# Kernel optimization log

Hardware: AMD Instinct MI355X
Metric: run time of the kernel (lower is better)

Reference implementation:

```python
import jax, jax.numpy as jnp
import numpy as np

NUM_GRAPHS = 1024  # fill_max for batch ids; fixed num_segments for jit


def setup_inputs() -> dict:
    key = jax.random.key(0)
    k1, k2 = jax.random.split(key)
    N, D = 1000000, 256
    x = jax.random.normal(k1, (N, D), dtype=jnp.float32)
    batch = jnp.sort(jax.random.randint(k2, (N,), 0, NUM_GRAPHS, dtype=jnp.int64))
    return {"input": x, "batch": batch}


def reference(input, batch):
    # per-node L2 norm over feature dim: [N]
    all_norms = jnp.sqrt(jnp.sum(input.astype(jnp.float32) ** 2, axis=1))
    seg = batch.astype(jnp.int32)
    # segment-reduce: sum of norms and node counts per graph, [NUM_GRAPHS]
    norm_sum = jax.ops.segment_sum(all_norms, seg, num_segments=NUM_GRAPHS)
    counts = jax.ops.segment_sum(jnp.ones_like(all_norms), seg, num_segments=NUM_GRAPHS)
    per_graph = jnp.where(counts > 0, norm_sum / counts, 0.0)
    # original loops b in range(batch.max()) -> graphs 0..max-1 only
    bmax = batch.max().astype(jnp.float32)
    mask = jnp.arange(NUM_GRAPHS, dtype=jnp.float32) < bmax
    norm_mean = jnp.sum(per_graph * mask) / (bmax + 1.0)
    # module returns input unchanged; norm_mean is the recorded statistic
    return input, norm_mean
```

## Files before the change

kernel.cpp:

```cpp
#include <hip/hip_runtime.h>

#define NUM_GRAPHS 1024
#define D 256

__global__ void activs_init_kernel(float* __restrict__ sums, float* __restrict__ cnts) {
    int i = blockIdx.x * blockDim.x + threadIdx.x;
    if (i < NUM_GRAPHS) {
        sums[i] = 0.0f;
        cnts[i] = 0.0f;
    }
}

__device__ __forceinline__ float sq4(const float4 v) {
    return v.x * v.x + v.y * v.y + v.z * v.z + v.w * v.w;
}

struct Rows8 {
    float4 v0, v1, v2, v3, v4, v5, v6, v7;
};

__device__ __forceinline__ void load8(Rows8& R, const float* __restrict__ x,
                                      int r, int lane) {
    R.v0 = ((const float4*)(x + (size_t)(r + 0) * D))[lane];
    R.v1 = ((const float4*)(x + (size_t)(r + 1) * D))[lane];
    R.v2 = ((const float4*)(x + (size_t)(r + 2) * D))[lane];
    R.v3 = ((const float4*)(x + (size_t)(r + 3) * D))[lane];
    R.v4 = ((const float4*)(x + (size_t)(r + 4) * D))[lane];
    R.v5 = ((const float4*)(x + (size_t)(r + 5) * D))[lane];
    R.v6 = ((const float4*)(x + (size_t)(r + 6) * D))[lane];
    R.v7 = ((const float4*)(x + (size_t)(r + 7) * D))[lane];
}

__device__ __forceinline__ void store8(const Rows8& R, float* __restrict__ out,
                                       int r, int lane) {
    ((float4*)(out + (size_t)(r + 0) * D))[lane] = R.v0;
    ((float4*)(out + (size_t)(r + 1) * D))[lane] = R.v1;
    ((float4*)(out + (size_t)(r + 2) * D))[lane] = R.v2;
    ((float4*)(out + (size_t)(r + 3) * D))[lane] = R.v3;
    ((float4*)(out + (size_t)(r + 4) * D))[lane] = R.v4;
    ((float4*)(out + (size_t)(r + 5) * D))[lane] = R.v5;
    ((float4*)(out + (size_t)(r + 6) * D))[lane] = R.v6;
    ((float4*)(out + (size_t)(r + 7) * D))[lane] = R.v7;
}

__global__ __launch_bounds__(256) void activs_stream_kernel(
        const float* __restrict__ x, float* __restrict__ out,
        float* __restrict__ norms, int N) {
    const int lane = threadIdx.x & 63;
    const int waveId = (blockIdx.x * blockDim.x + threadIdx.x) >> 6;
    const int totalWaves = (gridDim.x * blockDim.x) >> 6;
    const int stride = totalWaves * 8;

    const int Nq = N & ~7;

    int r = waveId * 8;
    if (r < Nq) {
        Rows8 cur;
        load8(cur, x, r, lane);

        while (true) {
            const int rn = r + stride;
            const bool more = (rn < Nq);
            Rows8 nxt;
            if (more) load8(nxt, x, rn, lane);

            store8(cur, out, r, lane);

            float s0 = sq4(cur.v0), s1 = sq4(cur.v1);
            float s2 = sq4(cur.v2), s3 = sq4(cur.v3);
            float s4 = sq4(cur.v4), s5 = sq4(cur.v5);
            float s6 = sq4(cur.v6), s7 = sq4(cur.v7);
            #pragma unroll
            for (int m = 1; m <= 32; m <<= 1) {
                s0 += __shfl_xor(s0, m, 64);
                s1 += __shfl_xor(s1, m, 64);
                s2 += __shfl_xor(s2, m, 64);
                s3 += __shfl_xor(s3, m, 64);
                s4 += __shfl_xor(s4, m, 64);
                s5 += __shfl_xor(s5, m, 64);
                s6 += __shfl_xor(s6, m, 64);
                s7 += __shfl_xor(s7, m, 64);
            }
            float nv = s0;
            nv = (lane == 1) ? s1 : nv;
            nv = (lane == 2) ? s2 : nv;
            nv = (lane == 3) ? s3 : nv;
            nv = (lane == 4) ? s4 : nv;
            nv = (lane == 5) ? s5 : nv;
            nv = (lane == 6) ? s6 : nv;
            nv = (lane == 7) ? s7 : nv;
            if (lane < 8) norms[r + lane] = sqrtf(nv);

            if (!more) break;
            cur = nxt;
            r = rn;
        }
    }

    if (waveId == 0) {
        for (int t = Nq; t < N; ++t) {
            const float4 v = ((const float4*)(x + (size_t)t * D))[lane];
            ((float4*)(out + (size_t)t * D))[lane] = v;
            float s = sq4(v);
            #pragma unroll
            for (int m = 32; m; m >>= 1) s += __shfl_xor(s, m, 64);
            if (lane == 0) norms[t] = sqrtf(s);
        }
    }
}

__global__ __launch_bounds__(256) void activs_segred_kernel(
        const float* __restrict__ norms, const int* __restrict__ batch,
        float* __restrict__ sums, float* __restrict__ cnts, int N) {
    __shared__ float lsum[NUM_GRAPHS];
    __shared__ float lcnt[NUM_GRAPHS];
    const int tid = threadIdx.x;

    for (int i = tid; i < NUM_GRAPHS; i += 256) {
        lsum[i] = 0.0f;
        lcnt[i] = 0.0f;
    }
    __syncthreads();

    const int base = blockIdx.x * 1024 + tid * 4;
    if (base < N) {
        const float4 nv = *(const float4*)(norms + base);
        const int4 bv = *(const int4*)(batch + base);
        const float n[4] = {nv.x, nv.y, nv.z, nv.w};
        const int b[4] = {bv.x, bv.y, bv.z, bv.w};
        int seg = b[0];
        float rs = n[0], rc = 1.0f;
        #pragma unroll
        for (int k = 1; k < 4; ++k) {
            if (b[k] == seg) { rs += n[k]; rc += 1.0f; }
            else {
                atomicAdd(&lsum[seg], rs);
                atomicAdd(&lcnt[seg], rc);
                seg = b[k]; rs = n[k]; rc = 1.0f;
            }
        }
        atomicAdd(&lsum[seg], rs);
        atomicAdd(&lcnt[seg], rc);
    }
    __syncthreads();

    for (int i = tid; i < NUM_GRAPHS; i += 256) {
        if (lcnt[i] != 0.0f) {
            atomicAdd(&sums[i], lsum[i]);
            atomicAdd(&cnts[i], lcnt[i]);
        }
    }
}

__global__ __launch_bounds__(256) void activs_fused_kernel(
        const float* __restrict__ x, const int* __restrict__ batch,
        float* __restrict__ out, float* __restrict__ sums,
        float* __restrict__ cnts, int N) {
    const int lane = threadIdx.x & 63;
    const int waveId = (blockIdx.x * blockDim.x + threadIdx.x) >> 6;
    const int totalWaves = (gridDim.x * blockDim.x) >> 6;
    const int stride = totalWaves * 8;
    const int Nq = N & ~7;

    int r = waveId * 8;
    if (r < Nq) {
        Rows8 cur;
        load8(cur, x, r, lane);
        int4 w0 = ((const int4*)(batch + r))[0];
        int4 w1 = ((const int4*)(batch + r))[1];

        while (true) {
            const int rn = r + stride;
            const bool more = (rn < Nq);
            Rows8 nxt;
            int4 nw0, nw1;
            if (more) {
                load8(nxt, x, rn, lane);
                nw0 = ((const int4*)(batch + rn))[0];
                nw1 = ((const int4*)(batch + rn))[1];
            }
            store8(cur, out, r, lane);

            float s0 = sq4(cur.v0), s1 = sq4(cur.v1);
            float s2 = sq4(cur.v2), s3 = sq4(cur.v3);
            float s4 = sq4(cur.v4), s5 = sq4(cur.v5);
            float s6 = sq4(cur.v6), s7 = sq4(cur.v7);
            #pragma unroll
            for (int m = 1; m <= 32; m <<= 1) {
                s0 += __shfl_xor(s0, m, 64);
                s1 += __shfl_xor(s1, m, 64);
                s2 += __shfl_xor(s2, m, 64);
                s3 += __shfl_xor(s3, m, 64);
                s4 += __shfl_xor(s4, m, 64);
                s5 += __shfl_xor(s5, m, 64);
                s6 += __shfl_xor(s6, m, 64);
                s7 += __shfl_xor(s7, m, 64);
            }

            if (lane == 0) {
                const float n[8] = {sqrtf(s0), sqrtf(s1), sqrtf(s2), sqrtf(s3),
                                    sqrtf(s4), sqrtf(s5), sqrtf(s6), sqrtf(s7)};
                const int b[8] = {w0.x, w0.y, w0.z, w0.w, w1.x, w1.y, w1.z, w1.w};
                int seg = b[0];
                float rs = n[0], rc = 1.0f;
                #pragma unroll
                for (int k = 1; k < 8; ++k) {
                    if (b[k] == seg) { rs += n[k]; rc += 1.0f; }
                    else {
                        atomicAdd(&sums[seg], rs);
                        atomicAdd(&cnts[seg], rc);
                        seg = b[k]; rs = n[k]; rc = 1.0f;
                    }
                }
                atomicAdd(&sums[seg], rs);
                atomicAdd(&cnts[seg], rc);
            }

            if (!more) break;
            cur = nxt; w0 = nw0; w1 = nw1; r = rn;
        }
    }
    if (waveId == 0) {
        for (int t = Nq; t < N; ++t) {
            const float4 v = ((const float4*)(x + (size_t)t * D))[lane];
            ((float4*)(out + (size_t)t * D))[lane] = v;
            float s = sq4(v);
            #pragma unroll
            for (int m = 32; m; m >>= 1) s += __shfl_xor(s, m, 64);
            if (lane == 0) {
                atomicAdd(&sums[batch[t]], sqrtf(s));
                atomicAdd(&cnts[batch[t]], 1.0f);
            }
        }
    }
}

__global__ __launch_bounds__(1024) void activs_finalize_kernel(
        const float* __restrict__ sums, const float* __restrict__ cnts,
        const int* __restrict__ batch, int N, float* __restrict__ out_scalar) {
    __shared__ float red[16];
    const int i = threadIdx.x;
    const int lane = i & 63;
    const int w = i >> 6;

    const float bmax = (float)batch[N - 1];

    float c = cnts[i];
    float pg = (c > 0.0f) ? (sums[i] / c) : 0.0f;
    float val = (((float)i) < bmax) ? pg : 0.0f;

    #pragma unroll
    for (int m = 32; m; m >>= 1) val += __shfl_xor(val, m, 64);
    if (lane == 0) red[w] = val;
    __syncthreads();

    if (w == 0) {
        float v = (lane < 16) ? red[lane] : 0.0f;
        #pragma unroll
        for (int m = 8; m; m >>= 1) v += __shfl_xor(v, m, 64);
        if (lane == 0) out_scalar[0] = v / (bmax + 1.0f);
    }
}

extern "C" void kernel_launch(void* const* d_in, const int* in_sizes, int n_in,
                              void* d_out, int out_size, void* d_ws, size_t ws_size,
                              hipStream_t stream) {
    const float* x = (const float*)d_in[0];
    const int* batch = (const int*)d_in[1];
    float* out = (float*)d_out;

    const int N = in_sizes[1];

    const size_t need_norm = ((size_t)N + 2 * NUM_GRAPHS) * sizeof(float);

    if (ws_size >= need_norm) {
        float* norms = (float*)d_ws;
        float* sums = norms + N;
        float* cnts = sums + NUM_GRAPHS;

        hipLaunchKernelGGL(activs_init_kernel, dim3(4), dim3(256), 0, stream, sums, cnts);
        hipLaunchKernelGGL(activs_stream_kernel, dim3(2048), dim3(256), 0, stream,
                           x, out, norms, N);
        hipLaunchKernelGGL(activs_segred_kernel, dim3((N + 1023) / 1024), dim3(256),
                           0, stream, norms, batch, sums, cnts, N);
        hipLaunchKernelGGL(activs_finalize_kernel, dim3(1), dim3(1024), 0, stream,
                           sums, cnts, batch, N, out + (size_t)N * D);
    } else {
        float* sums = (float*)d_ws;
        float* cnts = sums + NUM_GRAPHS;

        hipLaunchKernelGGL(activs_init_kernel, dim3(4), dim3(256), 0, stream, sums, cnts);
        hipLaunchKernelGGL(activs_fused_kernel, dim3(2048), dim3(256), 0, stream,
                           x, batch, out, sums, cnts, N);
        hipLaunchKernelGGL(activs_finalize_kernel, dim3(1), dim3(1024), 0, stream,
                           sums, cnts, batch, N, out + (size_t)N * D);
    }
}
```

Baseline: 403.4 us.

## Stage input rows through LDS via direct global-to-LDS loads in stream kernel

Replaces the register double-buffered streaming kernel with a tile-per-block kernel that uses global_load_lds to move 32 rows into shared memory, then reads them back to copy to the output and compute row norms. The aim is to bypass VGPR staging for the loads and cut register pressure. In exchange it drops the software prefetch of the next rows and adds two block barriers per tile, so load and store overlap now depends on occupancy (32 KB of LDS per block).

```diff
diff --git a/kernel.cpp b/kernel.cpp
--- a/kernel.cpp
+++ b/kernel.cpp
@@ -2,6 +2,7 @@
 
 #define NUM_GRAPHS 1024
 #define D 256
+#define TILE_ROWS 32
 
 __global__ void activs_init_kernel(float* __restrict__ sums, float* __restrict__ cnts) {
     int i = blockIdx.x * blockDim.x + threadIdx.x;
@@ -15,90 +16,80 @@
     return v.x * v.x + v.y * v.y + v.z * v.z + v.w * v.w;
 }
 
-struct Rows8 {
-    float4 v0, v1, v2, v3, v4, v5, v6, v7;
-};
-
-__device__ __forceinline__ void load8(Rows8& R, const float* __restrict__ x,
-                                      int r, int lane) {
-    R.v0 = ((const float4*)(x + (size_t)(r + 0) * D))[lane];
-    R.v1 = ((const float4*)(x + (size_t)(r + 1) * D))[lane];
-    R.v2 = ((const float4*)(x + (size_t)(r + 2) * D))[lane];
-    R.v3 = ((const float4*)(x + (size_t)(r + 3) * D))[lane];
-    R.v4 = ((const float4*)(x + (size_t)(r + 4) * D))[lane];
-    R.v5 = ((const float4*)(x + (size_t)(r + 5) * D))[lane];
-    R.v6 = ((const float4*)(x + (size_t)(r + 6) * D))[lane];
-    R.v7 = ((const float4*)(x + (size_t)(r + 7) * D))[lane];
-}
-
-__device__ __forceinline__ void store8(const Rows8& R, float* __restrict__ out,
-                                       int r, int lane) {
-    ((float4*)(out + (size_t)(r + 0) * D))[lane] = R.v0;
-    ((float4*)(out + (size_t)(r + 1) * D))[lane] = R.v1;
-    ((float4*)(out + (size_t)(r + 2) * D))[lane] = R.v2;
-    ((float4*)(out + (size_t)(r + 3) * D))[lane] = R.v3;
-    ((float4*)(out + (size_t)(r + 4) * D))[lane] = R.v4;
-    ((float4*)(out + (size_t)(r + 5) * D))[lane] = R.v5;
-    ((float4*)(out + (size_t)(r + 6) * D))[lane] = R.v6;
-    ((float4*)(out + (size_t)(r + 7) * D))[lane] = R.v7;
-}
-
-__global__ __launch_bounds__(256) void activs_stream_kernel(
+__device__ __forceinline__ void gload_lds16(const float* gsrc_lane, float* lds_base) {
+    __builtin_amdgcn_global_load_lds(
+        (const __attribute__((address_space(1))) void*)gsrc_lane,
+        (__attribute__((address_space(3))) void*)lds_base,
+        16, 0, 0);
+}
+
+__global__ __launch_bounds__(256) void activs_stage_kernel(
         const float* __restrict__ x, float* __restrict__ out,
         float* __restrict__ norms, int N) {
+    __shared__ float lds[TILE_ROWS * D];
+
     const int lane = threadIdx.x & 63;
-    const int waveId = (blockIdx.x * blockDim.x + threadIdx.x) >> 6;
-    const int totalWaves = (gridDim.x * blockDim.x) >> 6;
-    const int stride = totalWaves * 8;
-
-    const int Nq = N & ~7;
-
-    int r = waveId * 8;
-    if (r < Nq) {
-        Rows8 cur;
-        load8(cur, x, r, lane);
-
-        while (true) {
-            const int rn = r + stride;
-            const bool more = (rn < Nq);
-            Rows8 nxt;
-            if (more) load8(nxt, x, rn, lane);
-
-            store8(cur, out, r, lane);
-
-            float s0 = sq4(cur.v0), s1 = sq4(cur.v1);
-            float s2 = sq4(cur.v2), s3 = sq4(cur.v3);
-            float s4 = sq4(cur.v4), s5 = sq4(cur.v5);
-            float s6 = sq4(cur.v6), s7 = sq4(cur.v7);
-            #pragma unroll
-            for (int m = 1; m <= 32; m <<= 1) {
-                s0 += __shfl_xor(s0, m, 64);
-                s1 += __shfl_xor(s1, m, 64);
-                s2 += __shfl_xor(s2, m, 64);
-                s3 += __shfl_xor(s3, m, 64);
-                s4 += __shfl_xor(s4, m, 64);
-                s5 += __shfl_xor(s5, m, 64);
-                s6 += __shfl_xor(s6, m, 64);
-                s7 += __shfl_xor(s7, m, 64);
-            }
-            float nv = s0;
-            nv = (lane == 1) ? s1 : nv;
-            nv = (lane == 2) ? s2 : nv;
-            nv = (lane == 3) ? s3 : nv;
-            nv = (lane == 4) ? s4 : nv;
-            nv = (lane == 5) ? s5 : nv;
-            nv = (lane == 6) ? s6 : nv;
-            nv = (lane == 7) ? s7 : nv;
-            if (lane < 8) norms[r + lane] = sqrtf(nv);
-
-            if (!more) break;
-            cur = nxt;
-            r = rn;
-        }
-    }
-
-    if (waveId == 0) {
-        for (int t = Nq; t < N; ++t) {
+    const int w = threadIdx.x >> 6;
+    const int nTiles = N / TILE_ROWS;
+
+    for (int t = blockIdx.x; t < nTiles; t += gridDim.x) {
+        const int r0 = t * TILE_ROWS;
+
+        #pragma unroll
+        for (int j = 0; j < 8; ++j) {
+            const int rt = 8 * w + j;
+            gload_lds16(x + (size_t)(r0 + rt) * D + lane * 4, lds + rt * D);
+        }
+        __syncthreads();
+
+        float s0, s1, s2, s3, s4, s5, s6, s7;
+        {
+            const int rt = 8 * w;
+            float4 v;
+            v = ((const float4*)(lds + (rt + 0) * D))[lane];
+            ((float4*)(out + (size_t)(r0 + rt + 0) * D))[lane] = v; s0 = sq4(v);
+            v = ((const float4*)(lds + (rt + 1) * D))[lane];
+            ((float4*)(out + (size_t)(r0 + rt + 1) * D))[lane] = v; s1 = sq4(v);
+            v = ((const float4*)(lds + (rt + 2) * D))[lane];
+            ((float4*)(out + (size_t)(r0 + rt + 2) * D))[lane] = v; s2 = sq4(v);
+            v = ((const float4*)(lds + (rt + 3) * D))[lane];
+            ((float4*)(out + (size_t)(r0 + rt + 3) * D))[lane] = v; s3 = sq4(v);
+            v = ((const float4*)(lds + (rt + 4) * D))[lane];
+            ((float4*)(out + (size_t)(r0 + rt + 4) * D))[lane] = v; s4 = sq4(v);
+            v = ((const float4*)(lds + (rt + 5) * D))[lane];
+            ((float4*)(out + (size_t)(r0 + rt + 5) * D))[lane] = v; s5 = sq4(v);
+            v = ((const float4*)(lds + (rt + 6) * D))[lane];
+            ((float4*)(out + (size_t)(r0 + rt + 6) * D))[lane] = v; s6 = sq4(v);
+            v = ((const float4*)(lds + (rt + 7) * D))[lane];
+            ((float4*)(out + (size_t)(r0 + rt + 7) * D))[lane] = v; s7 = sq4(v);
+        }
+
+        #pragma unroll
+        for (int m = 1; m <= 32; m <<= 1) {
+            s0 += __shfl_xor(s0, m, 64);
+            s1 += __shfl_xor(s1, m, 64);
+            s2 += __shfl_xor(s2, m, 64);
+            s3 += __shfl_xor(s3, m, 64);
+            s4 += __shfl_xor(s4, m, 64);
+            s5 += __shfl_xor(s5, m, 64);
+            s6 += __shfl_xor(s6, m, 64);
+            s7 += __shfl_xor(s7, m, 64);
+        }
+        float nv = s0;
+        nv = (lane == 1) ? s1 : nv;
+        nv = (lane == 2) ? s2 : nv;
+        nv = (lane == 3) ? s3 : nv;
+        nv = (lane == 4) ? s4 : nv;
+        nv = (lane == 5) ? s5 : nv;
+        nv = (lane == 6) ? s6 : nv;
+        nv = (lane == 7) ? s7 : nv;
+        if (lane < 8) norms[r0 + 8 * w + lane] = sqrtf(nv);
+
+        __syncthreads();
+    }
+
+    if (blockIdx.x == 0 && w == 0) {
+        for (int t = nTiles * TILE_ROWS; t < N; ++t) {
             const float4 v = ((const float4*)(x + (size_t)t * D))[lane];
             ((float4*)(out + (size_t)t * D))[lane] = v;
             float s = sq4(v);
@@ -150,6 +141,34 @@
             atomicAdd(&cnts[i], lcnt[i]);
         }
     }
+}
+
+struct Rows8 {
+    float4 v0, v1, v2, v3, v4, v5, v6, v7;
+};
+
+__device__ __forceinline__ void load8(Rows8& R, const float* __restrict__ x,
+                                      int r, int lane) {
+    R.v0 = ((const float4*)(x + (size_t)(r + 0) * D))[lane];
+    R.v1 = ((const float4*)(x + (size_t)(r + 1) * D))[lane];
+    R.v2 = ((const float4*)(x + (size_t)(r + 2) * D))[lane];
+    R.v3 = ((const float4*)(x + (size_t)(r + 3) * D))[lane];
+    R.v4 = ((const float4*)(x + (size_t)(r + 4) * D))[lane];
+    R.v5 = ((const float4*)(x + (size_t)(r + 5) * D))[lane];
+    R.v6 = ((const float4*)(x + (size_t)(r + 6) * D))[lane];
+    R.v7 = ((const float4*)(x + (size_t)(r + 7) * D))[lane];
+}
+
+__device__ __forceinline__ void store8(const Rows8& R, float* __restrict__ out,
+                                       int r, int lane) {
+    ((float4*)(out + (size_t)(r + 0) * D))[lane] = R.v0;
+    ((float4*)(out + (size_t)(r + 1) * D))[lane] = R.v1;
+    ((float4*)(out + (size_t)(r + 2) * D))[lane] = R.v2;
+    ((float4*)(out + (size_t)(r + 3) * D))[lane] = R.v3;
+    ((float4*)(out + (size_t)(r + 4) * D))[lane] = R.v4;
+    ((float4*)(out + (size_t)(r + 5) * D))[lane] = R.v5;
+    ((float4*)(out + (size_t)(r + 6) * D))[lane] = R.v6;
+    ((float4*)(out + (size_t)(r + 7) * D))[lane] = R.v7;
 }
 
 __global__ __launch_bounds__(256) void activs_fused_kernel(
@@ -279,7 +298,7 @@
         float* cnts = sums + NUM_GRAPHS;
 
         hipLaunchKernelGGL(activs_init_kernel, dim3(4), dim3(256), 0, stream, sums, cnts);
-        hipLaunchKernelGGL(activs_stream_kernel, dim3(2048), dim3(256), 0, stream,
+        hipLaunchKernelGGL(activs_stage_kernel, dim3(2048), dim3(256), 0, stream,
                            x, out, norms, N);
         hipLaunchKernelGGL(activs_segred_kernel, dim3((N + 1023) / 1024), dim3(256),
                            0, stream, norms, batch, sums, cnts, N);
```

Result: no change. 408.2 us (+1.2%).
